# Kernel tuning notes

Measured on AMD Instinct MI355X. Metric: run time of the kernel, lower is better.

Reference implementation:

```python
import jax, jax.numpy as jnp
import numpy as np

N_EMBD = 768
N_HEAD = 12
B, T = 4, 2048
EPS = 1e-5


def layernorm(x, w, b):
    mu = jnp.mean(x, axis=-1, keepdims=True)
    var = jnp.mean(jnp.square(x - mu), axis=-1, keepdims=True)
    return (x - mu) * jax.lax.rsqrt(var + EPS) * w + b


def setup_inputs() -> dict:
    key = jax.random.key(0)
    ks = jax.random.split(key, 6)
    C = N_EMBD
    s = 0.02
    return {
        "x": jax.random.normal(ks[0], (B, T, C), jnp.float32),
        "ln1_w": jnp.ones((C,), jnp.float32),
        "ln1_b": jnp.zeros((C,), jnp.float32),
        "W_qkv": jax.random.normal(ks[1], (C, 3 * C), jnp.float32) * s,
        "b_qkv": jnp.zeros((3 * C,), jnp.float32),
        "W_attnproj": jax.random.normal(ks[2], (C, C), jnp.float32) * s,
        "b_attnproj": jnp.zeros((C,), jnp.float32),
        "ln2_w": jnp.ones((C,), jnp.float32),
        "ln2_b": jnp.zeros((C,), jnp.float32),
        "W_fc": jax.random.normal(ks[3], (C, 4 * C), jnp.float32) * s,
        "b_fc": jnp.zeros((4 * C,), jnp.float32),
        "W_mlpproj": jax.random.normal(ks[4], (4 * C, C), jnp.float32) * s,
        "b_mlpproj": jnp.zeros((C,), jnp.float32),
    }


def reference(x, ln1_w, ln1_b, W_qkv, b_qkv, W_attnproj, b_attnproj,
              ln2_w, ln2_b, W_fc, b_fc, W_mlpproj, b_mlpproj):
    Bx, Tx, C = x.shape
    H = N_HEAD
    Dh = C // H

    # --- attention branch ---
    h = layernorm(x, ln1_w, ln1_b)
    qkv = h @ W_qkv + b_qkv                       # [B, T, 3C]
    q, k, v = jnp.split(qkv, 3, axis=-1)
    q = q.reshape(Bx, Tx, H, Dh).transpose(0, 2, 1, 3)  # [B, H, T, Dh]
    k = k.reshape(Bx, Tx, H, Dh).transpose(0, 2, 1, 3)
    v = v.reshape(Bx, Tx, H, Dh).transpose(0, 2, 1, 3)
    att = jnp.einsum('bhqd,bhkd->bhqk', q, k) * (1.0 / np.sqrt(Dh))
    att = jax.nn.softmax(att, axis=-1)            # full softmax attention (no mask)
    y = jnp.einsum('bhqk,bhkd->bhqd', att, v)     # [B, H, T, Dh]
    y = y.transpose(0, 2, 1, 3).reshape(Bx, Tx, C)
    y = y @ W_attnproj + b_attnproj
    x = x + y

    # --- MLP branch ---
    h = layernorm(x, ln2_w, ln2_b)
    h = jax.nn.gelu(h @ W_fc + b_fc, approximate=False)
    h = h @ W_mlpproj + b_mlpproj
    return x + h
```

## Files before the change

### kernel.cpp

```cpp
#include <hip/hip_runtime.h>

typedef __bf16 bf16x8 __attribute__((ext_vector_type(8)));
typedef __bf16 bf16x4 __attribute__((ext_vector_type(4)));
typedef float f32x4 __attribute__((ext_vector_type(4)));
typedef unsigned short u16;
typedef unsigned long long u64;

#define GL2LDS(gp, lp) __builtin_amdgcn_global_load_lds(                      \
    (const __attribute__((address_space(1))) void*)(gp),                      \
    (__attribute__((address_space(3))) void*)(lp), 16, 0, 0)

__device__ __forceinline__ u16 f2u(float f) {
    __bf16 h = (__bf16)f;
    return __builtin_bit_cast(u16, h);
}

__device__ __forceinline__ float fexp2(float x) {
    float r;
    asm("v_exp_f32 %0, %1" : "=v"(r) : "v"(x));
    return r;
}

__device__ __forceinline__ float frcp(float x) {
    float r;
    asm("v_rcp_f32 %0, %1" : "=v"(r) : "v"(x));
    return r;
}

__device__ __forceinline__ float gelu(float x) {
    const float a = x * x;
    const float b = fmaf(a, 0.10294323f, 2.30220795f);
    const float u = fexp2(x * b);
    const float r = frcp(1.0f + u);
    return (x > 8.0f) ? x : x * u * r;
}

template <int N>
__device__ __forceinline__ void waitv() {
    if constexpr (N == 0) asm volatile("s_waitcnt vmcnt(0)" ::: "memory");
    else if constexpr (N == 4) asm volatile("s_waitcnt vmcnt(4)" ::: "memory");
    else if constexpr (N == 6) asm volatile("s_waitcnt vmcnt(6)" ::: "memory");
    else if constexpr (N == 8) asm volatile("s_waitcnt vmcnt(8)" ::: "memory");
}

__device__ __forceinline__ f32x4 mfma16(bf16x8 a, bf16x8 b, f32x4 c) {
    return __builtin_amdgcn_mfma_f32_16x16x32_bf16(a, b, c, 0, 0, 0);
}

__global__ __launch_bounds__(256) void transpose_kernel(
    const float* __restrict__ W, u16* __restrict__ Wt, int K, int N) {
    __shared__ float tile[32][33];
    const int tx = threadIdx.x & 31, ty = threadIdx.x >> 5;
    const int n0 = blockIdx.x * 32, k0 = blockIdx.y * 32;
#pragma unroll
    for (int i = 0; i < 4; i++)
        tile[ty + 8 * i][tx] = W[(size_t)(k0 + ty + 8 * i) * N + n0 + tx];
    __syncthreads();
#pragma unroll
    for (int i = 0; i < 4; i++)
        Wt[(size_t)(n0 + ty + 8 * i) * K + k0 + tx] = f2u(tile[tx][ty + 8 * i]);
}

__global__ __launch_bounds__(256) void ln_kernel(
    const float* __restrict__ xin, const float* __restrict__ wgt,
    const float* __restrict__ bia, u16* __restrict__ outp) {
    const int row = blockIdx.x, t = threadIdx.x;
    const float* xr = xin + (size_t)row * 768;
    float v0 = xr[t], v1 = xr[t + 256], v2 = xr[t + 512];
    float s = v0 + v1 + v2;
    float ss = v0 * v0 + v1 * v1 + v2 * v2;
#pragma unroll
    for (int off = 32; off; off >>= 1) {
        s += __shfl_xor(s, off);
        ss += __shfl_xor(ss, off);
    }
    __shared__ float red[8];
    const int w = t >> 6;
    if ((t & 63) == 0) { red[w] = s; red[4 + w] = ss; }
    __syncthreads();
    s  = red[0] + red[1] + red[2] + red[3];
    ss = red[4] + red[5] + red[6] + red[7];
    const float mu = s * (1.f / 768.f);
    const float var = ss * (1.f / 768.f) - mu * mu;
    const float rs = rsqrtf(var + 1e-5f);
    u16* orow = outp + (size_t)row * 768;
    orow[t]       = f2u((v0 - mu) * rs * wgt[t]       + bia[t]);
    orow[t + 256] = f2u((v1 - mu) * rs * wgt[t + 256] + bia[t + 256]);
    orow[t + 512] = f2u((v2 - mu) * rs * wgt[t + 512] + bia[t + 512]);
}

template <int EPI>
__global__ __launch_bounds__(256, 2) void gemm128(
    const u16* __restrict__ A, const u16* __restrict__ Bt,
    const float* __restrict__ bias, void* __restrict__ outp,
    u16* __restrict__ vt, int M, int N, int K) {
    __shared__ __align__(16) u16 As[2][8192];
    __shared__ __align__(16) u16 Bs[2][8192];
    const int t = threadIdx.x;
    const int lane = t & 63, w = t >> 6;
    const int wg0 = blockIdx.y * gridDim.x + blockIdx.x;
    const int xcd = wg0 & 7, loc = wg0 >> 3;
    const int gx = gridDim.x;
    const int m0 = (xcd * 8 + loc / gx) * 128;
    const int n0 = (loc % gx) * 128;
    const int wm = (w >> 1) * 64, wn = (w & 1) * 64;
    const int lq = lane & 15, g = lane >> 4;

    f32x4 acc[4][4];
#pragma unroll
    for (int i = 0; i < 4; i++)
#pragma unroll
        for (int j = 0; j < 4; j++) acc[i][j] = (f32x4){0.f, 0.f, 0.f, 0.f};

    const int srow8 = w * 8 + (lane >> 3);
    const int scol = ((lane & 7) ^ (lane >> 3)) * 8;
    const u16* gA_[4];
    const u16* gB_[4];
#pragma unroll
    for (int a = 0; a < 4; a++) {
        gA_[a] = A + (size_t)(m0 + a * 32 + srow8) * K + scol;
        gB_[a] = Bt + (size_t)(n0 + a * 32 + srow8) * K + scol;
    }
    const int KT = K >> 6;

#define STAGE128(buf, kt)                                                     \
    do {                                                                      \
        const int ko_ = (kt) << 6;                                            \
        _Pragma("unroll")                                                     \
        for (int a = 0; a < 4; a++) {                                         \
            GL2LDS(gA_[a] + ko_, (char*)As[buf] + a * 4096 + w * 1024);       \
            GL2LDS(gB_[a] + ko_, (char*)Bs[buf] + a * 4096 + w * 1024);       \
        }                                                                     \
    } while (0)

    STAGE128(0, 0);
    STAGE128(1, 1);
    for (int kt = 0; kt < KT; ++kt) {
        if (kt + 1 < KT) waitv<8>(); else waitv<0>();
        __builtin_amdgcn_s_barrier();
        __builtin_amdgcn_sched_barrier(0);
        const char* aB = (char*)As[kt & 1] + (wm + lq) * 128;
        const char* bB = (char*)Bs[kt & 1] + (wn + lq) * 128;
        const int sw = lq & 7;
#pragma unroll
        for (int s = 0; s < 2; s++) {
            const int co = (((s << 2) + g) ^ sw) << 4;
            bf16x8 af[4], bfr[4];
#pragma unroll
            for (int m = 0; m < 4; m++)
                af[m] = *(const bf16x8*)(aB + m * 2048 + co);
#pragma unroll
            for (int n = 0; n < 4; n++)
                bfr[n] = *(const bf16x8*)(bB + n * 2048 + co);
            __builtin_amdgcn_s_setprio(1);
#pragma unroll
            for (int m = 0; m < 4; m++)
#pragma unroll
                for (int n = 0; n < 4; n++)
                    acc[m][n] = mfma16(af[m], bfr[n], acc[m][n]);
            __builtin_amdgcn_s_setprio(0);
        }
        __builtin_amdgcn_sched_barrier(0);
        __builtin_amdgcn_s_barrier();
        if (kt + 2 < KT) STAGE128(kt & 1, kt + 2);
    }
#undef STAGE128

#pragma unroll
    for (int n = 0; n < 4; n++) {
        const int col = n0 + wn + 16 * n + lq;
        const float bv = bias[col];
#pragma unroll
        for (int m = 0; m < 4; m++) {
            const int rbase = m0 + wm + 16 * m + 4 * g;
            if constexpr (EPI == 0) {
                if (col < 1536) {
                    const float qs = (col < 768) ? 0.18033688f : 1.0f;
#pragma unroll
                    for (int r = 0; r < 4; r++) {
                        const size_t idx = (size_t)(rbase + r) * N + col;
                        ((u16*)outp)[idx] = f2u((acc[m][n][r] + bv) * qs);
                    }
                } else {
                    const int d = col - 1536;
                    bf16x4 pk;
#pragma unroll
                    for (int r = 0; r < 4; r++)
                        pk[r] = (__bf16)(acc[m][n][r] + bv);
                    u16* vrow = vt +
                        ((size_t)((rbase >> 11) * 12 + (d >> 6)) * 64 + (d & 63)) * 2048 +
                        (rbase & 2047);
                    *(u64*)vrow = __builtin_bit_cast(u64, pk);
                }
            } else {
#pragma unroll
                for (int r = 0; r < 4; r++) {
                    const size_t idx = (size_t)(rbase + r) * N + col;
                    ((u16*)outp)[idx] = f2u(gelu(acc[m][n][r] + bv));
                }
            }
        }
    }
}

__global__ __launch_bounds__(256, 3) void gemm_k64(
    const u16* __restrict__ A, const u16* __restrict__ Bt,
    const float* __restrict__ bias, const float* __restrict__ res,
    float* __restrict__ outp, int M, int N, int K) {
    __shared__ __align__(16) u16 As[2][4096];
    __shared__ __align__(16) u16 Bs[2][8192];
    const int t = threadIdx.x;
    const int lane = t & 63, w = t >> 6;
    const int wg0 = blockIdx.y * gridDim.x + blockIdx.x;
    const int xcd = wg0 & 7, loc = wg0 >> 3;
    const int gx = gridDim.x, gy = gridDim.y;
    const int m0 = (xcd * (gy >> 3) + loc / gx) * 64;
    const int n0 = (loc % gx) * 128;
    const int wm = (w >> 1) * 32, wn = (w & 1) * 64;
    const int lq = lane & 15, g = lane >> 4;

    f32x4 acc[2][4];
#pragma unroll
    for (int i = 0; i < 2; i++)
#pragma unroll
        for (int j = 0; j < 4; j++) acc[i][j] = (f32x4){0.f, 0.f, 0.f, 0.f};

    const int srow8 = w * 8 + (lane >> 3);
    const int scol = ((lane & 7) ^ (lane >> 3)) * 8;
    const u16* gA_0 = A + (size_t)(m0 + srow8) * K + scol;
    const u16* gA_1 = A + (size_t)(m0 + 32 + srow8) * K + scol;
    const u16* gB_0 = Bt + (size_t)(n0 + srow8) * K + scol;
    const u16* gB_1 = Bt + (size_t)(n0 + 32 + srow8) * K + scol;
    const u16* gB_2 = Bt + (size_t)(n0 + 64 + srow8) * K + scol;
    const u16* gB_3 = Bt + (size_t)(n0 + 96 + srow8) * K + scol;

    const int KT = K >> 6;

#define STAGE64(buf, kt)                                                      \
    do {                                                                      \
        const int ko_ = (kt) << 6;                                            \
        GL2LDS(gA_0 + ko_, (char*)As[buf] + w * 1024);                        \
        GL2LDS(gA_1 + ko_, (char*)As[buf] + 4096 + w * 1024);                 \
        GL2LDS(gB_0 + ko_, (char*)Bs[buf] + w * 1024);                        \
        GL2LDS(gB_1 + ko_, (char*)Bs[buf] + 4096 + w * 1024);                 \
        GL2LDS(gB_2 + ko_, (char*)Bs[buf] + 8192 + w * 1024);                 \
        GL2LDS(gB_3 + ko_, (char*)Bs[buf] + 12288 + w * 1024);                \
    } while (0)

    STAGE64(0, 0);
    STAGE64(1, 1);
    for (int kt = 0; kt < KT; ++kt) {
        if (kt + 1 < KT) waitv<6>(); else waitv<0>();
        __builtin_amdgcn_s_barrier();
        __builtin_amdgcn_sched_barrier(0);
        const char* aB = (char*)As[kt & 1] + (wm + lq) * 128;
        const char* bB = (char*)Bs[kt & 1] + (wn + lq) * 128;
        const int sw = lq & 7;
#pragma unroll
        for (int s = 0; s < 2; s++) {
            const int co = (((s << 2) + g) ^ sw) << 4;
            bf16x8 af[2], bfr[4];
#pragma unroll
            for (int m = 0; m < 2; m++)
                af[m] = *(const bf16x8*)(aB + m * 2048 + co);
#pragma unroll
            for (int n = 0; n < 4; n++)
                bfr[n] = *(const bf16x8*)(bB + n * 2048 + co);
            __builtin_amdgcn_s_setprio(1);
#pragma unroll
            for (int m = 0; m < 2; m++)
#pragma unroll
                for (int n = 0; n < 4; n++)
                    acc[m][n] = mfma16(af[m], bfr[n], acc[m][n]);
            __builtin_amdgcn_s_setprio(0);
        }
        __builtin_amdgcn_sched_barrier(0);
        __builtin_amdgcn_s_barrier();
        if (kt + 2 < KT) STAGE64(kt & 1, kt + 2);
    }
#undef STAGE64

#pragma unroll
    for (int n = 0; n < 4; n++) {
        const int col = n0 + wn + 16 * n + lq;
        const float bv = bias[col];
#pragma unroll
        for (int m = 0; m < 2; m++) {
            const int rbase = m0 + wm + 16 * m + 4 * g;
#pragma unroll
            for (int r = 0; r < 4; r++) {
                const size_t idx = (size_t)(rbase + r) * N + col;
                outp[idx] = acc[m][n][r] + bv + res[idx];
            }
        }
    }
}

__global__ __launch_bounds__(256, 3) void attn_kernel(
    const u16* __restrict__ qkv, const u16* __restrict__ Vt,
    u16* __restrict__ y) {
    __shared__ __align__(16) u16 Ks[2][4096];
    __shared__ __align__(16) u16 Vts[2][4096];
    __shared__ __align__(16) u16 Ps[4][2048];
    const int t = threadIdx.x, lane = t & 63, w = t >> 6;
    int wg = blockIdx.y * gridDim.x + blockIdx.x;
    wg = (wg & 7) * ((gridDim.x * gridDim.y) >> 3) + (wg >> 3);
    const int bh = wg / gridDim.x;
    const int b = bh / 12, h = bh % 12;
    const int q0 = (wg % gridDim.x) * 128 + w * 32;
    const int lq = lane & 15, g = lane >> 4;
    const int swz = (lq & 7) << 4;

    bf16x8 qf[2][2];
#pragma unroll
    for (int qh = 0; qh < 2; qh++) {
        const u16* qp =
            qkv + (size_t)(b * 2048 + q0 + qh * 16 + lq) * 2304 + h * 64 + g * 8;
        qf[qh][0] = *(const bf16x8*)(qp);
        qf[qh][1] = *(const bf16x8*)(qp + 32);
    }
    bf16x8 ones;
#pragma unroll
    for (int i = 0; i < 8; i++) ones[i] = (__bf16)1.0f;

    f32x4 acc_o[2][4], acc_s[2];
#pragma unroll
    for (int qh = 0; qh < 2; qh++) {
        acc_s[qh] = (f32x4){0.f, 0.f, 0.f, 0.f};
#pragma unroll
        for (int f = 0; f < 4; f++) acc_o[qh][f] = (f32x4){0.f, 0.f, 0.f, 0.f};
    }

    const int srow = t >> 3, sc = (t & 7) ^ (srow & 7);
    const u16* kg = qkv + 768 + h * 64 + sc * 8 + (size_t)(b * 2048 + srow) * 2304;
    const u16* vg = Vt + (size_t)(bh * 64 + srow) * 2048 + sc * 8;

#define STAGEKV(buf, kt)                                                      \
    do {                                                                      \
        const int kn_ = (kt) * 64;                                            \
        GL2LDS(kg + (size_t)kn_ * 2304, (char*)Ks[buf] + w * 1024);           \
        GL2LDS(kg + (size_t)(kn_ + 32) * 2304,                                \
               (char*)Ks[buf] + w * 1024 + 4096);                             \
        GL2LDS(vg + kn_, (char*)Vts[buf] + w * 1024);                         \
        GL2LDS(vg + 32 * 2048 + kn_, (char*)Vts[buf] + w * 1024 + 4096);      \
    } while (0)

    STAGEKV(0, 0);
    STAGEKV(1, 1);
    for (int kt = 0; kt < 32; ++kt) {
        const int buf = kt & 1;
        if (kt + 1 < 32) waitv<4>(); else waitv<0>();
        __builtin_amdgcn_s_barrier();
        __builtin_amdgcn_sched_barrier(0);
        const char* KB = (const char*)Ks[buf];
        const char* VB = (const char*)Vts[buf];

        f32x4 st[2][4];
        __builtin_amdgcn_s_setprio(1);
#pragma unroll
        for (int kb = 0; kb < 4; kb++) {
            st[0][kb] = (f32x4){0.f, 0.f, 0.f, 0.f};
            st[1][kb] = (f32x4){0.f, 0.f, 0.f, 0.f};
            const char* kr = KB + (kb * 16 + lq) * 128;
#pragma unroll
            for (int dh = 0; dh < 2; dh++) {
                const bf16x8 kf =
                    *(const bf16x8*)(kr + ((((dh << 2) + g) << 4) ^ swz));
                st[0][kb] = mfma16(kf, qf[0][dh], st[0][kb]);
                st[1][kb] = mfma16(kf, qf[1][dh], st[1][kb]);
            }
        }
        __builtin_amdgcn_s_setprio(0);

#pragma unroll
        for (int qh = 0; qh < 2; qh++) {
            char* pw = (char*)Ps[w] + (qh * 16 + lq) * 128 + ((g & 1) << 3);
#pragma unroll
            for (int kb = 0; kb < 4; kb++) {
                bf16x4 pb;
#pragma unroll
                for (int r = 0; r < 4; r++)
                    pb[r] = (__bf16)fexp2(st[qh][kb][r]);
                *(u64*)(pw + ((((kb << 1) + (g >> 1)) << 4) ^ swz)) =
                    __builtin_bit_cast(u64, pb);
            }
        }

        __builtin_amdgcn_s_setprio(1);
#pragma unroll
        for (int kk = 0; kk < 2; kk++) {
            const int co = ((kk << 2) + g) << 4;
            bf16x8 vf[4];
#pragma unroll
            for (int f = 0; f < 4; f++)
                vf[f] = *(const bf16x8*)(VB + (16 * f + lq) * 128 + (co ^ swz));
#pragma unroll
            for (int qh = 0; qh < 2; qh++) {
                const bf16x8 pf = *(const bf16x8*)(
                    (const char*)Ps[w] + (qh * 16 + lq) * 128 + (co ^ swz));
#pragma unroll
                for (int f = 0; f < 4; f++)
                    acc_o[qh][f] = mfma16(vf[f], pf, acc_o[qh][f]);
                acc_s[qh] = mfma16(ones, pf, acc_s[qh]);
            }
        }
        __builtin_amdgcn_s_setprio(0);
        __builtin_amdgcn_sched_barrier(0);
        __builtin_amdgcn_s_barrier();
        if (kt + 2 < 32) STAGEKV(buf, kt + 2);
    }
#undef STAGEKV

#pragma unroll
    for (int qh = 0; qh < 2; qh++) {
        const float rinv = frcp(acc_s[qh][0]);
        char* yb = (char*)(y + (size_t)(b * 2048 + q0 + qh * 16 + lq) * 768 +
                           h * 64);
#pragma unroll
    for (int f = 0; f < 4; f++) {
            bf16x4 pk;
#pragma unroll
            for (int r = 0; r < 4; r++) pk[r] = (__bf16)(acc_o[qh][f][r] * rinv);
            *(u64*)(yb + f * 32 + g * 8) = __builtin_bit_cast(u64, pk);
        }
    }
}

extern "C" void kernel_launch(void* const* d_in, const int* in_sizes, int n_in,
                              void* d_out, int out_size, void* d_ws,
                              size_t ws_size, hipStream_t stream) {
    const float* x    = (const float*)d_in[0];
    const float* ln1w = (const float*)d_in[1];
    const float* ln1b = (const float*)d_in[2];
    const float* Wqkv = (const float*)d_in[3];
    const float* bqkv = (const float*)d_in[4];
    const float* Wap  = (const float*)d_in[5];
    const float* bap  = (const float*)d_in[6];
    const float* ln2w = (const float*)d_in[7];
    const float* ln2b = (const float*)d_in[8];
    const float* Wfc  = (const float*)d_in[9];
    const float* bfc  = (const float*)d_in[10];
    const float* Wmp  = (const float*)d_in[11];
    const float* bmp  = (const float*)d_in[12];
    float* out = (float*)d_out;

    char* ws = (char*)d_ws;
    u16* Wt_qkv = (u16*)(ws);
    u16* Wt_ap  = (u16*)(ws + 3538944);
    u16* Wt_fc  = (u16*)(ws + 4718592);
    u16* Wt_mp  = (u16*)(ws + 9437184);
    u16* bufA   = (u16*)(ws + 14155776);
    u16* bufB   = (u16*)(ws + 26738688);
    u16* VtBuf  = (u16*)(ws + 64487424);

    transpose_kernel<<<dim3(72, 24), 256, 0, stream>>>(Wqkv, Wt_qkv, 768, 2304);
    transpose_kernel<<<dim3(24, 24), 256, 0, stream>>>(Wap, Wt_ap, 768, 768);
    transpose_kernel<<<dim3(96, 24), 256, 0, stream>>>(Wfc, Wt_fc, 768, 3072);
    transpose_kernel<<<dim3(24, 96), 256, 0, stream>>>(Wmp, Wt_mp, 3072, 768);

    ln_kernel<<<8192, 256, 0, stream>>>(x, ln1w, ln1b, bufA);
    gemm128<0><<<dim3(18, 64), 256, 0, stream>>>(
        bufA, Wt_qkv, bqkv, bufB, VtBuf, 8192, 2304, 768);
    attn_kernel<<<dim3(16, 48), 256, 0, stream>>>(bufB, VtBuf, bufA);
    gemm_k64<<<dim3(6, 128), 256, 0, stream>>>(
        bufA, Wt_ap, bap, x, out, 8192, 768, 768);
    ln_kernel<<<8192, 256, 0, stream>>>(out, ln2w, ln2b, bufA);
    gemm128<2><<<dim3(24, 64), 256, 0, stream>>>(
        bufA, Wt_fc, bfc, bufB, nullptr, 8192, 3072, 768);
    gemm_k64<<<dim3(6, 128), 256, 0, stream>>>(
        bufB, Wt_mp, bmp, out, out, 8192, 768, 3072);
}
```

Measured before the change: 269.9 us.

## Widen QKV and FC GEMM tiles to 128x256 with a K=32 stage

Replaces the 128x128 GEMM used for the QKV and FC projections with a 128x256 tile. Each wave now computes 64x128, and the K step per stage drops from 64 to 32, with a new LDS swizzle and fewer async global-to-LDS loads per stage. The aim is more MFMA work per LDS fragment load and half as many blocks, so A is re-read less. The costs are twice the accumulator registers (128 floats per thread), which could pressure occupancy at 2 blocks per CU, and twice as many barriers because K steps are smaller. The grid also shrinks to 576 or 768 blocks, which may leave the CUs less evenly loaded.

```diff
diff --git a/kernel.cpp b/kernel.cpp
--- a/kernel.cpp
+++ b/kernel.cpp
@@ -40,7 +40,6 @@
     if constexpr (N == 0) asm volatile("s_waitcnt vmcnt(0)" ::: "memory");
     else if constexpr (N == 4) asm volatile("s_waitcnt vmcnt(4)" ::: "memory");
     else if constexpr (N == 6) asm volatile("s_waitcnt vmcnt(6)" ::: "memory");
-    else if constexpr (N == 8) asm volatile("s_waitcnt vmcnt(8)" ::: "memory");
 }
 
 __device__ __forceinline__ f32x4 mfma16(bf16x8 a, bf16x8 b, f32x4 c) {
@@ -90,84 +89,79 @@
 }
 
 template <int EPI>
-__global__ __launch_bounds__(256, 2) void gemm128(
+__global__ __launch_bounds__(256, 2) void gemm_w(
     const u16* __restrict__ A, const u16* __restrict__ Bt,
     const float* __restrict__ bias, void* __restrict__ outp,
     u16* __restrict__ vt, int M, int N, int K) {
-    __shared__ __align__(16) u16 As[2][8192];
+    __shared__ __align__(16) u16 As[2][4096];
     __shared__ __align__(16) u16 Bs[2][8192];
     const int t = threadIdx.x;
     const int lane = t & 63, w = t >> 6;
     const int wg0 = blockIdx.y * gridDim.x + blockIdx.x;
     const int xcd = wg0 & 7, loc = wg0 >> 3;
-    const int gx = gridDim.x;
-    const int m0 = (xcd * 8 + loc / gx) * 128;
-    const int n0 = (loc % gx) * 128;
-    const int wm = (w >> 1) * 64, wn = (w & 1) * 64;
+    const int gx = gridDim.x, gy = gridDim.y;
+    const int m0 = (xcd * (gy >> 3) + loc / gx) * 128;
+    const int n0 = (loc % gx) * 256;
+    const int wm = (w >> 1) * 64, wn = (w & 1) * 128;
     const int lq = lane & 15, g = lane >> 4;
 
-    f32x4 acc[4][4];
+    f32x4 acc[4][8];
 #pragma unroll
     for (int i = 0; i < 4; i++)
 #pragma unroll
-        for (int j = 0; j < 4; j++) acc[i][j] = (f32x4){0.f, 0.f, 0.f, 0.f};
-
-    const int srow8 = w * 8 + (lane >> 3);
-    const int scol = ((lane & 7) ^ (lane >> 3)) * 8;
-    const u16* gA_[4];
-    const u16* gB_[4];
-#pragma unroll
-    for (int a = 0; a < 4; a++) {
-        gA_[a] = A + (size_t)(m0 + a * 32 + srow8) * K + scol;
-        gB_[a] = Bt + (size_t)(n0 + a * 32 + srow8) * K + scol;
-    }
-    const int KT = K >> 6;
-
-#define STAGE128(buf, kt)                                                     \
+        for (int j = 0; j < 8; j++) acc[i][j] = (f32x4){0.f, 0.f, 0.f, 0.f};
+
+    const int srow = t >> 2;
+    const int scol = ((t & 3) ^ ((t >> 3) & 3)) * 8;
+    const u16* gA0 = A + (size_t)(m0 + srow) * K + scol;
+    const u16* gA1 = A + (size_t)(m0 + 64 + srow) * K + scol;
+    const u16* gB0 = Bt + (size_t)(n0 + srow) * K + scol;
+    const u16* gB1 = Bt + (size_t)(n0 + 64 + srow) * K + scol;
+    const u16* gB2 = Bt + (size_t)(n0 + 128 + srow) * K + scol;
+    const u16* gB3 = Bt + (size_t)(n0 + 192 + srow) * K + scol;
+
+    const int cph = (g ^ ((lq >> 1) & 3)) << 4;
+    const int KT = K >> 5;
+
+#define STAGEW(buf, kt)                                                       \
     do {                                                                      \
-        const int ko_ = (kt) << 6;                                            \
-        _Pragma("unroll")                                                     \
-        for (int a = 0; a < 4; a++) {                                         \
-            GL2LDS(gA_[a] + ko_, (char*)As[buf] + a * 4096 + w * 1024);       \
-            GL2LDS(gB_[a] + ko_, (char*)Bs[buf] + a * 4096 + w * 1024);       \
-        }                                                                     \
+        const int ko_ = (kt) << 5;                                            \
+        GL2LDS(gA0 + ko_, (char*)As[buf] + w * 1024);                         \
+        GL2LDS(gA1 + ko_, (char*)As[buf] + 4096 + w * 1024);                  \
+        GL2LDS(gB0 + ko_, (char*)Bs[buf] + w * 1024);                         \
+        GL2LDS(gB1 + ko_, (char*)Bs[buf] + 4096 + w * 1024);                  \
+        GL2LDS(gB2 + ko_, (char*)Bs[buf] + 8192 + w * 1024);                  \
+        GL2LDS(gB3 + ko_, (char*)Bs[buf] + 12288 + w * 1024);                 \
     } while (0)
 
-    STAGE128(0, 0);
-    STAGE128(1, 1);
+    STAGEW(0, 0);
+    STAGEW(1, 1);
     for (int kt = 0; kt < KT; ++kt) {
-        if (kt + 1 < KT) waitv<8>(); else waitv<0>();
-        __builtin_amdgcn_s_barrier();
-        __builtin_amdgcn_sched_barrier(0);
-        const char* aB = (char*)As[kt & 1] + (wm + lq) * 128;
-        const char* bB = (char*)Bs[kt & 1] + (wn + lq) * 128;
-        const int sw = lq & 7;
-#pragma unroll
-        for (int s = 0; s < 2; s++) {
-            const int co = (((s << 2) + g) ^ sw) << 4;
-            bf16x8 af[4], bfr[4];
+        if (kt + 1 < KT) waitv<6>(); else waitv<0>();
+        __builtin_amdgcn_s_barrier();
+        __builtin_amdgcn_sched_barrier(0);
+        const char* rA = (char*)As[kt & 1] + (wm + lq) * 64 + cph;
+        const char* rB = (char*)Bs[kt & 1] + (wn + lq) * 64 + cph;
+        bf16x8 af[4];
+#pragma unroll
+        for (int m = 0; m < 4; m++) af[m] = *(const bf16x8*)(rA + m * 1024);
+        __builtin_amdgcn_s_setprio(1);
+#pragma unroll
+        for (int n = 0; n < 8; n++) {
+            const bf16x8 bfr = *(const bf16x8*)(rB + n * 1024);
 #pragma unroll
             for (int m = 0; m < 4; m++)
-                af[m] = *(const bf16x8*)(aB + m * 2048 + co);
-#pragma unroll
-            for (int n = 0; n < 4; n++)
-                bfr[n] = *(const bf16x8*)(bB + n * 2048 + co);
-            __builtin_amdgcn_s_setprio(1);
-#pragma unroll
-            for (int m = 0; m < 4; m++)
-#pragma unroll
-                for (int n = 0; n < 4; n++)
-                    acc[m][n] = mfma16(af[m], bfr[n], acc[m][n]);
-            __builtin_amdgcn_s_setprio(0);
-        }
-        __builtin_amdgcn_sched_barrier(0);
-        __builtin_amdgcn_s_barrier();
-        if (kt + 2 < KT) STAGE128(kt & 1, kt + 2);
-    }
-#undef STAGE128
-
-#pragma unroll
-    for (int n = 0; n < 4; n++) {
+                acc[m][n] = mfma16(af[m], bfr, acc[m][n]);
+        }
+        __builtin_amdgcn_s_setprio(0);
+        __builtin_amdgcn_sched_barrier(0);
+        __builtin_amdgcn_s_barrier();
+        if (kt + 2 < KT) STAGEW(kt & 1, kt + 2);
+    }
+#undef STAGEW
+
+#pragma unroll
+    for (int n = 0; n < 8; n++) {
         const int col = n0 + wn + 16 * n + lq;
         const float bv = bias[col];
 #pragma unroll
@@ -417,7 +411,7 @@
         char* yb = (char*)(y + (size_t)(b * 2048 + q0 + qh * 16 + lq) * 768 +
                            h * 64);
 #pragma unroll
-    for (int f = 0; f < 4; f++) {
+        for (int f = 0; f < 4; f++) {
             bf16x4 pk;
 #pragma unroll
             for (int r = 0; r < 4; r++) pk[r] = (__bf16)(acc_o[qh][f][r] * rinv);
@@ -459,13 +453,13 @@
     transpose_kernel<<<dim3(24, 96), 256, 0, stream>>>(Wmp, Wt_mp, 3072, 768);
 
     ln_kernel<<<8192, 256, 0, stream>>>(x, ln1w, ln1b, bufA);
-    gemm128<0><<<dim3(18, 64), 256, 0, stream>>>(
+    gemm_w<0><<<dim3(9, 64), 256, 0, stream>>>(
         bufA, Wt_qkv, bqkv, bufB, VtBuf, 8192, 2304, 768);
     attn_kernel<<<dim3(16, 48), 256, 0, stream>>>(bufB, VtBuf, bufA);
     gemm_k64<<<dim3(6, 128), 256, 0, stream>>>(
         bufA, Wt_ap, bap, x, out, 8192, 768, 768);
     ln_kernel<<<8192, 256, 0, stream>>>(out, ln2w, ln2b, bufA);
-    gemm128<2><<<dim3(24, 64), 256, 0, stream>>>(
+    gemm_w<2><<<dim3(12, 64), 256, 0, stream>>>(
         bufA, Wt_fc, bfc, bufB, nullptr, 8192, 3072, 768);
     gemm_k64<<<dim3(6, 128), 256, 0, stream>>>(
         bufB, Wt_mp, bmp, out, out, 8192, 768, 3072);
```

Result: slower. 281.1 us (+4.1%).
